# Performance work log

Measured on AMD Instinct MI355X. Metric: run time of the kernel, lower is better.

## Reference

```python
import jax, jax.numpy as jnp
import numpy as np

C = 256
CQK = C // 8  # query/key channels from Conv2d(in_dim, in_dim//8, 1)


def _cross_attn(x, y, qw, qb, kw, kb, vw, vb, gamma):
    # x, y: [B, C, H, W]; 1x1 convs are channel matmuls
    B, Cc, H, W = x.shape
    N = H * W
    xf = x.reshape(B, Cc, N)
    yf = y.reshape(B, Cc, N)
    q = jnp.einsum('oc,bcn->bno', qw, xf) + qb  # [B, N, CQK]
    k = jnp.einsum('oc,bcn->bon', kw, yf) + kb[:, None]  # [B, CQK, N]
    energy = jnp.einsum('bnc,bcm->bnm', q, k)  # [B, N, N]
    attn = jax.nn.softmax(energy, axis=2)
    v = jnp.einsum('oc,bcn->bon', vw, yf) + vb[:, None]  # [B, C, N]
    out = jnp.einsum('bcm,bnm->bcn', v, attn)  # value @ attention^T
    out = out.reshape(B, Cc, H, W)
    return gamma * out + x


def setup_inputs() -> dict:
    key = jax.random.key(0)
    ks = jax.random.split(key, 16)
    B, H, W = 4, 64, 64
    s = 1.0 / np.sqrt(C)
    d = {
        'x': jax.random.normal(ks[0], (B, C, H, W), jnp.float32),
        'y': jax.random.normal(ks[1], (B, C, H, W), jnp.float32),
        'z': jax.random.normal(ks[2], (B, C, H, W), jnp.float32),
        'q1_w': jax.random.normal(ks[3], (CQK, C), jnp.float32) * s,
        'q1_b': jax.random.normal(ks[4], (CQK,), jnp.float32) * s,
        'k1_w': jax.random.normal(ks[5], (CQK, C), jnp.float32) * s,
        'k1_b': jax.random.normal(ks[6], (CQK,), jnp.float32) * s,
        'v1_w': jax.random.normal(ks[7], (C, C), jnp.float32) * s,
        'v1_b': jax.random.normal(ks[8], (C,), jnp.float32) * s,
        'gamma1': jax.random.normal(ks[9], (1,), jnp.float32) * 0.1,
        'q2_w': jax.random.normal(ks[10], (CQK, C), jnp.float32) * s,
        'q2_b': jax.random.normal(ks[11], (CQK,), jnp.float32) * s,
        'k2_w': jax.random.normal(ks[12], (CQK, C), jnp.float32) * s,
        'k2_b': jax.random.normal(ks[13], (CQK,), jnp.float32) * s,
        'v2_w': jax.random.normal(ks[14], (C, C), jnp.float32) * s,
        'v2_b': jax.random.normal(ks[15], (C,), jnp.float32) * s,
        'gamma2': jax.random.normal(jax.random.fold_in(key, 99), (1,), jnp.float32) * 0.1,
    }
    return d


def reference(x, y, z, q1_w, q1_b, k1_w, k1_b, v1_w, v1_b, gamma1,
              q2_w, q2_b, k2_w, k2_b, v2_w, v2_b, gamma2):
    out1 = _cross_attn(x, y, q1_w, q1_b, k1_w, k1_b, v1_w, v1_b, gamma1)
    out2 = _cross_attn(out1, z, q2_w, q2_b, k2_w, k2_b, v2_w, v2_b, gamma2)
    return out2
```

## Files before the change

### kernel.cpp

```cpp
#include <hip/hip_runtime.h>
#include <hip/hip_bf16.h>

#define NSEQ 4096
#define CDIM 256
#define CQKD 32
#define LOG2E 1.4426950408889634f

typedef float v4f __attribute__((ext_vector_type(4)));
typedef float v16f __attribute__((ext_vector_type(16)));
typedef short v8s __attribute__((ext_vector_type(8)));

__device__ __forceinline__ float exp2_(float x) { return exp2f(x); }

__device__ __forceinline__ unsigned short f2bf(float x) {
  unsigned u = __builtin_bit_cast(unsigned, x);
  unsigned r = (u + 0x7FFFu + ((u >> 16) & 1u)) >> 16;
  return (unsigned short)r;
}
__device__ __forceinline__ float bf2f(unsigned short s) {
  unsigned u = ((unsigned)s) << 16;
  return __builtin_bit_cast(float, u);
}
__device__ __forceinline__ unsigned int pack_bf16(float a, float b) {
#if __has_builtin(__builtin_amdgcn_cvt_pk_bf16_f32)
  typedef __bf16 v2bf __attribute__((ext_vector_type(2)));
  v2bf r = __builtin_amdgcn_cvt_pk_bf16_f32(a, b);
  return __builtin_bit_cast(unsigned int, r);
#else
  return ((unsigned)f2bf(b) << 16) | (unsigned)f2bf(a);
#endif
}

__device__ __forceinline__ void barrier_lds() {
  __asm__ __volatile__("s_waitcnt lgkmcnt(0)\n\ts_barrier" ::: "memory");
}

__global__ __launch_bounds__(256) void convw_kernel(
    const float* __restrict__ q1w, const float* __restrict__ k1w,
    const float* __restrict__ k2w, const float* __restrict__ q2w,
    const float* __restrict__ v1w, const float* __restrict__ v2w,
    unsigned short* __restrict__ W) {
  const int s = blockIdx.x * 256 + threadIdx.x;
  const float* src;
  int o, ch0;
  size_t obase;
  float scale = 1.0f;
  if (s < 3072) {
    const int wsel = s >> 10, r = s & 1023;
    src = wsel == 0 ? q1w : (wsel == 1 ? k1w : k2w);
    const int ot = r >> 9, cb = (r >> 6) & 7, lane = r & 63;
    o = ot * 16 + (lane & 15);
    ch0 = cb * 32 + ((lane >> 4) & 3) * 8;
    obase = (size_t)wsel * 8192 + (size_t)r * 8;
  } else if (s < 19456) {
    const int s2 = s - 3072, which = s2 >> 13, r = s2 & 8191;
    src = which == 0 ? v1w : v2w;
    const int ot = r >> 9, cb = (r >> 6) & 7, lane = r & 63;
    o = ot * 16 + (lane & 15);
    ch0 = cb * 32 + ((lane >> 4) & 3) * 8;
    obase = 32768 + (size_t)which * 65536 + (size_t)r * 8;
  } else {
    const int r = s - 19456;
    src = q2w;
    const int lane = r & 63;
    o = lane & 31;
    ch0 = (r >> 6) * 16 + (lane >> 5) * 8;
    obase = 24576 + (size_t)r * 8;
    scale = LOG2E;
  }
#pragma unroll
  for (int j = 0; j < 8; ++j)
    W[obase + j] = f2bf(src[o * CDIM + ch0 + j] * scale);
}

__global__ __launch_bounds__(256) void prep_kernel(
    const float* __restrict__ x, const float* __restrict__ y,
    const float* __restrict__ z, const unsigned short* __restrict__ Wbf,
    const float* __restrict__ q1b, const float* __restrict__ k1b,
    const float* __restrict__ k2b, const float* __restrict__ v1b,
    const float* __restrict__ v2b, unsigned short* __restrict__ Q1,
    unsigned short* __restrict__ K1, unsigned short* __restrict__ K2,
    unsigned short* __restrict__ V1, unsigned short* __restrict__ V2) {
  __shared__ unsigned short t[256][72];
  __shared__ unsigned short Kt[64][40];
  const int src = blockIdx.z;
  const float* in = src == 0 ? x : (src == 1 ? y : z);
  const int b = blockIdx.y;
  const int n0 = blockIdx.x * 64;
  const int tid = threadIdx.x, lane = tid & 63, w = tid >> 6;
  const int quad = lane >> 4, r15 = lane & 15, l31 = lane & 31, lh = lane >> 5;
  const float* ip = in + (size_t)(b * CDIM) * NSEQ + n0;
  {
    const int chb = tid >> 4, c4 = (tid & 15) * 4;
#pragma unroll
    for (int p = 0; p < 16; ++p) {
      const int ch = p * 16 + chb;
      float4 v = *(const float4*)(ip + (size_t)ch * NSEQ + c4);
      uint2 pk;
      pk.x = pack_bf16(v.x, v.y);
      pk.y = pack_bf16(v.z, v.w);
      *(uint2*)&t[ch][c4] = pk;
    }
  }
  __syncthreads();
  v8s af[8];
#pragma unroll
  for (int cb = 0; cb < 8; ++cb) {
    union { unsigned short e[8]; v8s v; } u;
#pragma unroll
    for (int j = 0; j < 8; ++j) u.e[j] = t[cb * 32 + quad * 8 + j][w * 16 + r15];
    af[cb] = u.v;
  }
  const int nt = blockIdx.x * 4 + w;
  const unsigned short* Wqk = Wbf + src * 8192;
  v4f a0 = {0.f, 0.f, 0.f, 0.f}, a1 = a0;
#pragma unroll
  for (int cb = 0; cb < 8; ++cb) {
    v8s b0 = *(const v8s*)(Wqk + (size_t)cb * 512 + lane * 8);
    v8s b1 = *(const v8s*)(Wqk + (size_t)(8 + cb) * 512 + lane * 8);
    a0 = __builtin_amdgcn_mfma_f32_16x16x32_bf16(af[cb], b0, a0, 0, 0, 0);
    a1 = __builtin_amdgcn_mfma_f32_16x16x32_bf16(af[cb], b1, a1, 0, 0, 0);
  }
  if (src == 0) {
#pragma unroll
    for (int r = 0; r < 4; ++r) {
      Q1[((size_t)b * NSEQ + nt * 16 + quad * 4 + r) * CQKD + r15] =
          f2bf((a0[r] + q1b[r15]) * LOG2E);
      Q1[((size_t)b * NSEQ + nt * 16 + quad * 4 + r) * CQKD + 16 + r15] =
          f2bf((a1[r] + q1b[16 + r15]) * LOG2E);
    }
    return;
  }
  const float* kbias = src == 1 ? k1b : k2b;
#pragma unroll
  for (int r = 0; r < 4; ++r) {
    Kt[w * 16 + quad * 4 + r][r15] = f2bf(a0[r] + kbias[r15]);
    Kt[w * 16 + quad * 4 + r][16 + r15] = f2bf(a1[r] + kbias[16 + r15]);
  }
  const unsigned short* Wv = Wbf + 32768 + (src - 1) * 65536;
  const float* vbias = src == 1 ? v1b : v2b;
  v4f vacc[16];
#pragma unroll
  for (int ot = 0; ot < 16; ++ot) vacc[ot] = (v4f){0.f, 0.f, 0.f, 0.f};
#pragma unroll
  for (int cb = 0; cb < 8; ++cb) {
    const v8s afc = af[cb];
#pragma unroll
    for (int ot = 0; ot < 16; ++ot) {
      v8s bf = *(const v8s*)(Wv + (size_t)(ot * 8 + cb) * 512 + lane * 8);
      vacc[ot] = __builtin_amdgcn_mfma_f32_16x16x32_bf16(afc, bf, vacc[ot], 0, 0, 0);
    }
  }
  __syncthreads();
#pragma unroll
  for (int ot = 0; ot < 16; ++ot) {
    const int ch = ot * 16 + r15;
    const float bv = vbias[ch];
    uint2 pk;
    pk.x = pack_bf16(vacc[ot][0] + bv, vacc[ot][1] + bv);
    pk.y = pack_bf16(vacc[ot][2] + bv, vacc[ot][3] + bv);
    *(uint2*)&t[ch][w * 16 + quad * 4] = pk;
  }
  {
    unsigned short* Kout = (src == 1 ? K1 : K2) + (size_t)b * (NSEQ / 16) * 512;
    *(v8s*)(Kout + ((size_t)nt * 64 + lane) * 8) = *(const v8s*)&Kt[w * 16 + r15][quad * 8];
  }
  __syncthreads();
  unsigned short* Vout = (src == 1 ? V1 : V2) + (size_t)b * (NSEQ / 16) * 8 * 512;
#pragma unroll
  for (int chb = 0; chb < 8; ++chb)
    *(v8s*)(Vout + (((size_t)nt * 8 + chb) * 64 + lane) * 8) =
        *(const v8s*)&t[chb * 32 + l31][w * 16 + lh * 8];
}

#define PSTR 136

__device__ __forceinline__ void attn_tile(
    const unsigned short* __restrict__ Kl, const unsigned short* __restrict__ Vl,
    unsigned short* __restrict__ P, const v8s qf[4], int w, int lane,
    int pbuf, int tn, const v8s kfu, const v8s* vfu, v8s& kfn, v8s* vfn,
    v16f acc[2], float lsum[4]) {
  const v4f vzero4 = {0.f, 0.f, 0.f, 0.f};
  const int quad = (lane >> 4) & 3, r15 = lane & 15;
  const int l31 = lane & 31, lh = lane >> 5;
  kfn = *(const v8s*)(Kl + (size_t)tn * 4096);
#pragma unroll
  for (int s = 0; s < 8; ++s)
    vfn[s] = *(const v8s*)(Vl + ((size_t)tn * 64 + s * 8) * 512);
  unsigned short* pw = P + pbuf * (64 * PSTR) + w * 16 + quad * 4;
#pragma unroll
  for (int qt = 0; qt < 4; ++qt) {
    v4f st = __builtin_amdgcn_mfma_f32_16x16x32_bf16(kfu, qf[qt], vzero4, 0, 0, 0);
    float e0 = exp2_(st[0]), e1 = exp2_(st[1]), e2 = exp2_(st[2]), e3 = exp2_(st[3]);
    lsum[qt] += (e0 + e1) + (e2 + e3);
    uint2 pk;
    pk.x = pack_bf16(e0, e1);
    pk.y = pack_bf16(e2, e3);
    *(uint2*)(pw + (qt * 16 + r15) * PSTR) = pk;
  }
  barrier_lds();
  const unsigned short* pb = P + pbuf * (64 * PSTR);
#pragma unroll
  for (int s = 0; s < 8; ++s) {
    v8s pf0 = *(const v8s*)(pb + (size_t)l31 * PSTR + s * 16 + lh * 8);
    v8s pf1 = *(const v8s*)(pb + (size_t)(32 + l31) * PSTR + s * 16 + lh * 8);
    acc[0] = __builtin_amdgcn_mfma_f32_32x32x16_bf16(vfu[s], pf0, acc[0], 0, 0, 0);
    acc[1] = __builtin_amdgcn_mfma_f32_32x32x16_bf16(vfu[s], pf1, acc[1], 0, 0, 0);
  }
}

__device__ __forceinline__ void attn_loop(
    const unsigned short* __restrict__ Kp, const unsigned short* __restrict__ Vp,
    unsigned short* __restrict__ P, const v8s qf[4], int w, int lane,
    v16f acc[2], float lsum[4]) {
  const unsigned short* Kl = Kp + (size_t)w * 512 + lane * 8;
  const unsigned short* Vl = Vp + (size_t)w * 512 + lane * 8;
  v8s kA, kB, vA[8], vB[8];
  kA = *(const v8s*)(Kl);
#pragma unroll
  for (int s = 0; s < 8; ++s) vA[s] = *(const v8s*)(Vl + (size_t)s * 8 * 512);
  for (int kt = 0; kt < 32; kt += 2) {
    attn_tile(Kl, Vl, P, qf, w, lane, 0, (kt + 1) & 31, kA, vA, kB, vB, acc, lsum);
    attn_tile(Kl, Vl, P, qf, w, lane, 1, (kt + 2) & 31, kB, vB, kA, vA, acc, lsum);
  }
}

__global__ __launch_bounds__(512, 2) void fused_attn_kernel(
    const unsigned short* __restrict__ Q1g, const unsigned short* __restrict__ K1g,
    const unsigned short* __restrict__ V1g, const unsigned short* __restrict__ K2g,
    const unsigned short* __restrict__ V2g, const unsigned short* __restrict__ W2g,
    const float* __restrict__ x, const float* __restrict__ q2b,
    const float* __restrict__ g1p, const float* __restrict__ g2p,
    float* __restrict__ outp) {
  __shared__ __align__(16) unsigned short P[2 * 64 * PSTR];
  __shared__ __align__(16) unsigned short out1T[64 * 264];
  __shared__ __align__(16) unsigned short q2s[64 * 32];
  __shared__ float lbuf[8][64];

  const int tid = threadIdx.x;
  const int lane = tid & 63;
  const int w = tid >> 6;
  const int quad = lane >> 4;
  const int r15 = lane & 15;
  const int l31 = lane & 31, lh = lane >> 5;
  const int b = blockIdx.x & 3;
  const int n0 = (blockIdx.x >> 2) * 64;

  const float g1 = g1p[0];
  const float g2 = g2p[0];

  const unsigned short* Qp  = Q1g + (size_t)b * NSEQ * CQKD;
  const unsigned short* K1p = K1g + (size_t)b * (NSEQ / 16) * 512;
  const unsigned short* K2p = K2g + (size_t)b * (NSEQ / 16) * 512;
  const unsigned short* V1p = V1g + (size_t)b * (NSEQ / 16) * 8 * 512;
  const unsigned short* V2p = V2g + (size_t)b * (NSEQ / 16) * 8 * 512;

  v8s qf[4];
#pragma unroll
  for (int qt = 0; qt < 4; ++qt)
    qf[qt] = *(const v8s*)(Qp + (n0 + qt * 16 + r15) * CQKD + quad * 8);

  v16f acc[2];
  float lsum[4] = {0.f, 0.f, 0.f, 0.f};
  acc[0] = (v16f)(0.f); acc[1] = (v16f)(0.f);

  attn_loop(K1p, V1p, P, qf, w, lane, acc, lsum);
#pragma unroll
  for (int qt = 0; qt < 4; ++qt) {
    lsum[qt] += __shfl_xor(lsum[qt], 16);
    lsum[qt] += __shfl_xor(lsum[qt], 32);
  }
  if (lane < 16) {
#pragma unroll
    for (int qt = 0; qt < 4; ++qt) lbuf[w][qt * 16 + lane] = lsum[qt];
  }
  __syncthreads();
  float rinv[2];
#pragma unroll
  for (int qh = 0; qh < 2; ++qh) {
    const int q = qh * 32 + l31;
    float d = 0.f;
#pragma unroll
    for (int ww = 0; ww < 8; ++ww) d += lbuf[ww][q];
    rinv[qh] = 1.0f / d;
  }
#pragma unroll
  for (int qh = 0; qh < 2; ++qh) {
    const int q = qh * 32 + l31;
#pragma unroll
    for (int rg = 0; rg < 4; ++rg) {
      const int c = w * 32 + 8 * rg + 4 * lh;
      float o0 = g1 * (acc[qh][rg * 4 + 0] * rinv[qh]) + x[((size_t)b * CDIM + c + 0) * NSEQ + n0 + q];
      float o1 = g1 * (acc[qh][rg * 4 + 1] * rinv[qh]) + x[((size_t)b * CDIM + c + 1) * NSEQ + n0 + q];
      float o2 = g1 * (acc[qh][rg * 4 + 2] * rinv[qh]) + x[((size_t)b * CDIM + c + 2) * NSEQ + n0 + q];
      float o3 = g1 * (acc[qh][rg * 4 + 3] * rinv[qh]) + x[((size_t)b * CDIM + c + 3) * NSEQ + n0 + q];
      uint2 pk;
      pk.x = pack_bf16(o0, o1);
      pk.y = pack_bf16(o2, o3);
      *(uint2*)(out1T + (size_t)q * 264 + c) = pk;
    }
  }
  __syncthreads();

  if (w < 2) {
    const int qh = w;
    v16f qacc = (v16f)(0.f);
#pragma unroll
    for (int s = 0; s < 16; ++s) {
      v8s af = *(const v8s*)(W2g + (size_t)(s * 64 + lane) * 8);
      v8s bf = *(const v8s*)(out1T + (size_t)(qh * 32 + l31) * 264 + s * 16 + lh * 8);
      qacc = __builtin_amdgcn_mfma_f32_32x32x16_bf16(af, bf, qacc, 0, 0, 0);
    }
#pragma unroll
    for (int rg = 0; rg < 4; ++rg) {
      const int o = 8 * rg + 4 * lh;
      uint2 pk;
      pk.x = pack_bf16(qacc[rg * 4 + 0] + q2b[o + 0] * LOG2E, qacc[rg * 4 + 1] + q2b[o + 1] * LOG2E);
      pk.y = pack_bf16(qacc[rg * 4 + 2] + q2b[o + 2] * LOG2E, qacc[rg * 4 + 3] + q2b[o + 3] * LOG2E);
      *(uint2*)(q2s + (size_t)(qh * 32 + l31) * 32 + o) = pk;
    }
  }
  __syncthreads();

#pragma unroll
  for (int qt = 0; qt < 4; ++qt)
    qf[qt] = *(const v8s*)(q2s + (qt * 16 + r15) * 32 + quad * 8);
  acc[0] = (v16f)(0.f); acc[1] = (v16f)(0.f);
#pragma unroll
  for (int qt = 0; qt < 4; ++qt) lsum[qt] = 0.f;
  attn_loop(K2p, V2p, P, qf, w, lane, acc, lsum);
#pragma unroll
  for (int qt = 0; qt < 4; ++qt) {
    lsum[qt] += __shfl_xor(lsum[qt], 16);
    lsum[qt] += __shfl_xor(lsum[qt], 32);
  }
  __syncthreads();
  if (lane < 16) {
#pragma unroll
    for (int qt = 0; qt < 4; ++qt) lbuf[w][qt * 16 + lane] = lsum[qt];
  }
  __syncthreads();
#pragma unroll
  for (int qh = 0; qh < 2; ++qh) {
    const int q = qh * 32 + l31;
    float d = 0.f;
#pragma unroll
    for (int ww = 0; ww < 8; ++ww) d += lbuf[ww][q];
    rinv[qh] = 1.0f / d;
  }
#pragma unroll
  for (int qh = 0; qh < 2; ++qh) {
    const int q = qh * 32 + l31;
#pragma unroll
    for (int rg = 0; rg < 4; ++rg) {
      const int c = w * 32 + 8 * rg + 4 * lh;
#pragma unroll
      for (int i = 0; i < 4; ++i) {
        float res = bf2f(out1T[(size_t)q * 264 + c + i]);
        outp[((size_t)b * CDIM + c + i) * NSEQ + n0 + q] =
            g2 * (acc[qh][rg * 4 + i] * rinv[qh]) + res;
      }
    }
  }
}

extern "C" void kernel_launch(void* const* d_in, const int* in_sizes, int n_in,
                              void* d_out, int out_size, void* d_ws, size_t ws_size,
                              hipStream_t stream) {
  const float* x   = (const float*)d_in[0];
  const float* y   = (const float*)d_in[1];
  const float* z   = (const float*)d_in[2];
  const float* q1w = (const float*)d_in[3];
  const float* q1b = (const float*)d_in[4];
  const float* k1w = (const float*)d_in[5];
  const float* k1b = (const float*)d_in[6];
  const float* v1w = (const float*)d_in[7];
  const float* v1b = (const float*)d_in[8];
  const float* g1  = (const float*)d_in[9];
  const float* q2w = (const float*)d_in[10];
  const float* q2b = (const float*)d_in[11];
  const float* k2w = (const float*)d_in[12];
  const float* k2b = (const float*)d_in[13];
  const float* v2w = (const float*)d_in[14];
  const float* v2b = (const float*)d_in[15];
  const float* g2  = (const float*)d_in[16];
  char* ws = (char*)d_ws;
  unsigned short* Wbf = (unsigned short*)(ws);
  unsigned short* Q1  = (unsigned short*)(ws + 327680);
  unsigned short* K1  = (unsigned short*)(ws + 1376256);
  unsigned short* K2  = (unsigned short*)(ws + 2424832);
  unsigned short* V1  = (unsigned short*)(ws + 3473408);
  unsigned short* V2  = (unsigned short*)(ws + 11862016);
  float* outp = (float*)d_out;

  convw_kernel<<<dim3(80), 256, 0, stream>>>(q1w, k1w, k2w, q2w, v1w, v2w, Wbf);
  prep_kernel<<<dim3(64, 4, 3), 256, 0, stream>>>(x, y, z, Wbf, q1b, k1b, k2b, v1b,
                                                  v2b, Q1, K1, K2, V1, V2);
  fused_attn_kernel<<<dim3(256), 512, 0, stream>>>(Q1, K1, V1, K2, V2, Wbf + 24576, x,
                                                   q2b, g1, g2, outp);
}
```

Measured before the change: 237.2 us.

## Switch P·V matmul to FP8 with a max-subtraction pre-pass

Stores V and the softmax probabilities P as FP8 e4m3 and runs the P·V product with FP8 MFMA instructions instead of BF16, halving V global traffic and P LDS traffic. FP8 range is narrow, so a separate pass over the keys first computes the per-query row max, which is subtracted before exp2. exp2 now uses the hardware intrinsic. This adds a full extra QK pass per attention stage and lowers the precision of the probabilities and values, which risks accuracy tolerance.

```diff
diff --git a/kernel.cpp b/kernel.cpp
--- a/kernel.cpp
+++ b/kernel.cpp
@@ -9,8 +9,17 @@
 typedef float v4f __attribute__((ext_vector_type(4)));
 typedef float v16f __attribute__((ext_vector_type(16)));
 typedef short v8s __attribute__((ext_vector_type(8)));
-
-__device__ __forceinline__ float exp2_(float x) { return exp2f(x); }
+typedef unsigned long long u64;
+
+__device__ __forceinline__ float exp2_(float x) {
+#if __has_builtin(__builtin_amdgcn_exp2f)
+  return __builtin_amdgcn_exp2f(x);
+#else
+  float r;
+  __asm__("v_exp_f32 %0, %1" : "=v"(r) : "v"(x));
+  return r;
+#endif
+}
 
 __device__ __forceinline__ unsigned short f2bf(float x) {
   unsigned u = __builtin_bit_cast(unsigned, x);
@@ -28,6 +37,35 @@
   return __builtin_bit_cast(unsigned int, r);
 #else
   return ((unsigned)f2bf(b) << 16) | (unsigned)f2bf(a);
+#endif
+}
+
+__device__ __forceinline__ unsigned char f2e4m3(float x) {
+  unsigned u = __builtin_bit_cast(unsigned, x);
+  unsigned s = (u >> 24) & 0x80u;
+  unsigned au = u & 0x7fffffffu;
+  if (au > 0x43e00000u) return (unsigned char)(s | 0x7eu);
+  if (au < 0x3c800000u) {
+    float ax = __builtin_bit_cast(float, au);
+    int q = (int)(ax * 512.0f + 0.5f);
+    if (q > 7) q = 7;
+    return (unsigned char)(s | (unsigned)q);
+  }
+  int e = (int)((au >> 23) & 0xffu) - 127 + 7;
+  unsigned m = au & 0x7fffffu;
+  unsigned mr = m + 0x7ffffu + ((m >> 20) & 1u);
+  if (mr >= 0x800000u) { mr -= 0x800000u; e += 1; if (e >= 16) return (unsigned char)(s | 0x7e); }
+  return (unsigned char)(s | ((unsigned)e << 3) | (mr >> 20));
+}
+__device__ __forceinline__ unsigned int pack4_fp8(float a, float b, float c, float d) {
+#if __has_builtin(__builtin_amdgcn_cvt_pk_fp8_f32)
+  int v = 0;
+  v = __builtin_amdgcn_cvt_pk_fp8_f32(a, b, v, false);
+  v = __builtin_amdgcn_cvt_pk_fp8_f32(c, d, v, true);
+  return (unsigned int)v;
+#else
+  return (unsigned)f2e4m3(a) | ((unsigned)f2e4m3(b) << 8) |
+         ((unsigned)f2e4m3(c) << 16) | ((unsigned)f2e4m3(d) << 24);
 #endif
 }
 
@@ -80,7 +118,7 @@
     const float* __restrict__ k2b, const float* __restrict__ v1b,
     const float* __restrict__ v2b, unsigned short* __restrict__ Q1,
     unsigned short* __restrict__ K1, unsigned short* __restrict__ K2,
-    unsigned short* __restrict__ V1, unsigned short* __restrict__ V2) {
+    unsigned char* __restrict__ V1, unsigned char* __restrict__ V2) {
   __shared__ unsigned short t[256][72];
   __shared__ unsigned short Kt[64][40];
   const int src = blockIdx.z;
@@ -152,33 +190,69 @@
     }
   }
   __syncthreads();
+  unsigned char* Vt8 = (unsigned char*)t;
 #pragma unroll
   for (int ot = 0; ot < 16; ++ot) {
     const int ch = ot * 16 + r15;
     const float bv = vbias[ch];
-    uint2 pk;
-    pk.x = pack_bf16(vacc[ot][0] + bv, vacc[ot][1] + bv);
-    pk.y = pack_bf16(vacc[ot][2] + bv, vacc[ot][3] + bv);
-    *(uint2*)&t[ch][w * 16 + quad * 4] = pk;
+    *(unsigned int*)&Vt8[(size_t)ch * 72 + w * 16 + quad * 4] =
+        pack4_fp8(vacc[ot][0] + bv, vacc[ot][1] + bv, vacc[ot][2] + bv, vacc[ot][3] + bv);
   }
   {
     unsigned short* Kout = (src == 1 ? K1 : K2) + (size_t)b * (NSEQ / 16) * 512;
     *(v8s*)(Kout + ((size_t)nt * 64 + lane) * 8) = *(const v8s*)&Kt[w * 16 + r15][quad * 8];
   }
   __syncthreads();
-  unsigned short* Vout = (src == 1 ? V1 : V2) + (size_t)b * (NSEQ / 16) * 8 * 512;
+  unsigned char* Vout = (src == 1 ? V1 : V2) + (size_t)b * (NSEQ / 16) * 8 * 512;
 #pragma unroll
   for (int chb = 0; chb < 8; ++chb)
-    *(v8s*)(Vout + (((size_t)nt * 8 + chb) * 64 + lane) * 8) =
-        *(const v8s*)&t[chb * 32 + l31][w * 16 + lh * 8];
-}
-
-#define PSTR 136
+    *(u64*)(Vout + (((size_t)nt * 8 + chb) * 64 + lane) * 8) =
+        *(const u64*)&Vt8[(size_t)(chb * 32 + l31) * 72 + w * 16 + lh * 8];
+}
+
+
+__device__ __forceinline__ void max_pass(
+    const unsigned short* __restrict__ Kp, const v8s qf[4], int w, int lane,
+    float (*lbuf)[64], float m[4]) {
+  const v4f vzero4 = {0.f, 0.f, 0.f, 0.f};
+  const int r15 = lane & 15;
+  const unsigned short* Kl = Kp + (size_t)w * 512 + lane * 8;
+  v8s kA = *(const v8s*)(Kl);
+#pragma unroll
+  for (int qt = 0; qt < 4; ++qt) m[qt] = -3.0e38f;
+  for (int kt = 0; kt < 32; ++kt) {
+    v8s kB = *(const v8s*)(Kl + (size_t)((kt + 1) & 31) * 4096);
+#pragma unroll
+    for (int qt = 0; qt < 4; ++qt) {
+      v4f st = __builtin_amdgcn_mfma_f32_16x16x32_bf16(kA, qf[qt], vzero4, 0, 0, 0);
+      m[qt] = fmaxf(m[qt], fmaxf(fmaxf(st[0], st[1]), fmaxf(st[2], st[3])));
+    }
+    kA = kB;
+  }
+#pragma unroll
+  for (int qt = 0; qt < 4; ++qt) {
+    m[qt] = fmaxf(m[qt], __shfl_xor(m[qt], 16));
+    m[qt] = fmaxf(m[qt], __shfl_xor(m[qt], 32));
+  }
+  if (lane < 16) {
+#pragma unroll
+    for (int qt = 0; qt < 4; ++qt) lbuf[w][qt * 16 + lane] = m[qt];
+  }
+  __syncthreads();
+#pragma unroll
+  for (int qt = 0; qt < 4; ++qt) {
+    float mm = lbuf[0][qt * 16 + r15];
+#pragma unroll
+    for (int ww = 1; ww < 8; ++ww) mm = fmaxf(mm, lbuf[ww][qt * 16 + r15]);
+    m[qt] = mm;
+  }
+  __syncthreads();
+}
 
 __device__ __forceinline__ void attn_tile(
-    const unsigned short* __restrict__ Kl, const unsigned short* __restrict__ Vl,
-    unsigned short* __restrict__ P, const v8s qf[4], int w, int lane,
-    int pbuf, int tn, const v8s kfu, const v8s* vfu, v8s& kfn, v8s* vfn,
+    const unsigned short* __restrict__ Kl, const unsigned char* __restrict__ Vl,
+    unsigned char* __restrict__ P, const v8s qf[4], const float m[4], int w, int lane,
+    int pbuf, int tn, const v8s kfu, const u64* vfu, v8s& kfn, u64* vfn,
     v16f acc[2], float lsum[4]) {
   const v4f vzero4 = {0.f, 0.f, 0.f, 0.f};
   const int quad = (lane >> 4) & 3, r15 = lane & 15;
@@ -186,53 +260,52 @@
   kfn = *(const v8s*)(Kl + (size_t)tn * 4096);
 #pragma unroll
   for (int s = 0; s < 8; ++s)
-    vfn[s] = *(const v8s*)(Vl + ((size_t)tn * 64 + s * 8) * 512);
-  unsigned short* pw = P + pbuf * (64 * PSTR) + w * 16 + quad * 4;
+    vfn[s] = *(const u64*)(Vl + (size_t)tn * 32768 + s * 4096);
+  unsigned char* pw = P + pbuf * 8704 + w * 16 + quad * 4;
 #pragma unroll
   for (int qt = 0; qt < 4; ++qt) {
     v4f st = __builtin_amdgcn_mfma_f32_16x16x32_bf16(kfu, qf[qt], vzero4, 0, 0, 0);
-    float e0 = exp2_(st[0]), e1 = exp2_(st[1]), e2 = exp2_(st[2]), e3 = exp2_(st[3]);
+    float e0 = exp2_(st[0] - m[qt]), e1 = exp2_(st[1] - m[qt]);
+    float e2 = exp2_(st[2] - m[qt]), e3 = exp2_(st[3] - m[qt]);
     lsum[qt] += (e0 + e1) + (e2 + e3);
-    uint2 pk;
-    pk.x = pack_bf16(e0, e1);
-    pk.y = pack_bf16(e2, e3);
-    *(uint2*)(pw + (qt * 16 + r15) * PSTR) = pk;
+    *(unsigned int*)(pw + (size_t)(qt * 16 + r15) * 136) = pack4_fp8(e0, e1, e2, e3);
   }
   barrier_lds();
-  const unsigned short* pb = P + pbuf * (64 * PSTR);
+  const unsigned char* pb = P + pbuf * 8704;
 #pragma unroll
   for (int s = 0; s < 8; ++s) {
-    v8s pf0 = *(const v8s*)(pb + (size_t)l31 * PSTR + s * 16 + lh * 8);
-    v8s pf1 = *(const v8s*)(pb + (size_t)(32 + l31) * PSTR + s * 16 + lh * 8);
-    acc[0] = __builtin_amdgcn_mfma_f32_32x32x16_bf16(vfu[s], pf0, acc[0], 0, 0, 0);
-    acc[1] = __builtin_amdgcn_mfma_f32_32x32x16_bf16(vfu[s], pf1, acc[1], 0, 0, 0);
+    long pf0 = (long)*(const u64*)(pb + (size_t)l31 * 136 + s * 16 + lh * 8);
+    long pf1 = (long)*(const u64*)(pb + (size_t)(32 + l31) * 136 + s * 16 + lh * 8);
+    acc[0] = __builtin_amdgcn_mfma_f32_32x32x16_fp8_fp8((long)vfu[s], pf0, acc[0], 0, 0, 0);
+    acc[1] = __builtin_amdgcn_mfma_f32_32x32x16_fp8_fp8((long)vfu[s], pf1, acc[1], 0, 0, 0);
   }
 }
 
 __device__ __forceinline__ void attn_loop(
-    const unsigned short* __restrict__ Kp, const unsigned short* __restrict__ Vp,
-    unsigned short* __restrict__ P, const v8s qf[4], int w, int lane,
+    const unsigned short* __restrict__ Kp, const unsigned char* __restrict__ Vp,
+    unsigned char* __restrict__ P, const v8s qf[4], const float m[4], int w, int lane,
     v16f acc[2], float lsum[4]) {
   const unsigned short* Kl = Kp + (size_t)w * 512 + lane * 8;
-  const unsigned short* Vl = Vp + (size_t)w * 512 + lane * 8;
-  v8s kA, kB, vA[8], vB[8];
+  const unsigned char* Vl = Vp + (size_t)w * 512 + lane * 8;
+  v8s kA, kB;
+  u64 vA[8], vB[8];
   kA = *(const v8s*)(Kl);
 #pragma unroll
-  for (int s = 0; s < 8; ++s) vA[s] = *(const v8s*)(Vl + (size_t)s * 8 * 512);
+  for (int s = 0; s < 8; ++s) vA[s] = *(const u64*)(Vl + (size_t)s * 4096);
   for (int kt = 0; kt < 32; kt += 2) {
-    attn_tile(Kl, Vl, P, qf, w, lane, 0, (kt + 1) & 31, kA, vA, kB, vB, acc, lsum);
-    attn_tile(Kl, Vl, P, qf, w, lane, 1, (kt + 2) & 31, kB, vB, kA, vA, acc, lsum);
+    attn_tile(Kl, Vl, P, qf, m, w, lane, 0, (kt + 1) & 31, kA, vA, kB, vB, acc, lsum);
+    attn_tile(Kl, Vl, P, qf, m, w, lane, 1, (kt + 2) & 31, kB, vB, kA, vA, acc, lsum);
   }
 }
 
 __global__ __launch_bounds__(512, 2) void fused_attn_kernel(
     const unsigned short* __restrict__ Q1g, const unsigned short* __restrict__ K1g,
-    const unsigned short* __restrict__ V1g, const unsigned short* __restrict__ K2g,
-    const unsigned short* __restrict__ V2g, const unsigned short* __restrict__ W2g,
+    const unsigned char* __restrict__ V1g, const unsigned short* __restrict__ K2g,
+    const unsigned char* __restrict__ V2g, const unsigned short* __restrict__ W2g,
     const float* __restrict__ x, const float* __restrict__ q2b,
     const float* __restrict__ g1p, const float* __restrict__ g2p,
     float* __restrict__ outp) {
-  __shared__ __align__(16) unsigned short P[2 * 64 * PSTR];
+  __shared__ __align__(16) unsigned char P[2 * 8704];
   __shared__ __align__(16) unsigned short out1T[64 * 264];
   __shared__ __align__(16) unsigned short q2s[64 * 32];
   __shared__ float lbuf[8][64];
@@ -252,8 +325,8 @@
   const unsigned short* Qp  = Q1g + (size_t)b * NSEQ * CQKD;
   const unsigned short* K1p = K1g + (size_t)b * (NSEQ / 16) * 512;
   const unsigned short* K2p = K2g + (size_t)b * (NSEQ / 16) * 512;
-  const unsigned short* V1p = V1g + (size_t)b * (NSEQ / 16) * 8 * 512;
-  const unsigned short* V2p = V2g + (size_t)b * (NSEQ / 16) * 8 * 512;
+  const unsigned char* V1p  = V1g + (size_t)b * (NSEQ / 16) * 8 * 512;
+  const unsigned char* V2p  = V2g + (size_t)b * (NSEQ / 16) * 8 * 512;
 
   v8s qf[4];
 #pragma unroll
@@ -262,14 +335,17 @@
 
   v16f acc[2];
   float lsum[4] = {0.f, 0.f, 0.f, 0.f};
+  float m[4];
   acc[0] = (v16f)(0.f); acc[1] = (v16f)(0.f);
 
-  attn_loop(K1p, V1p, P, qf, w, lane, acc, lsum);
+  max_pass(K1p, qf, w, lane, lbuf, m);
+  attn_loop(K1p, V1p, P, qf, m, w, lane, acc, lsum);
 #pragma unroll
   for (int qt = 0; qt < 4; ++qt) {
     lsum[qt] += __shfl_xor(lsum[qt], 16);
     lsum[qt] += __shfl_xor(lsum[qt], 32);
   }
+  __syncthreads();
   if (lane < 16) {
 #pragma unroll
     for (int qt = 0; qt < 4; ++qt) lbuf[w][qt * 16 + lane] = lsum[qt];
@@ -328,7 +404,8 @@
   acc[0] = (v16f)(0.f); acc[1] = (v16f)(0.f);
 #pragma unroll
   for (int qt = 0; qt < 4; ++qt) lsum[qt] = 0.f;
-  attn_loop(K2p, V2p, P, qf, w, lane, acc, lsum);
+  max_pass(K2p, qf, w, lane, lbuf, m);
+  attn_loop(K2p, V2p, P, qf, m, w, lane, acc, lsum);
 #pragma unroll
   for (int qt = 0; qt < 4; ++qt) {
     lsum[qt] += __shfl_xor(lsum[qt], 16);
@@ -389,8 +466,8 @@
   unsigned short* Q1  = (unsigned short*)(ws + 327680);
   unsigned short* K1  = (unsigned short*)(ws + 1376256);
   unsigned short* K2  = (unsigned short*)(ws + 2424832);
-  unsigned short* V1  = (unsigned short*)(ws + 3473408);
-  unsigned short* V2  = (unsigned short*)(ws + 11862016);
+  unsigned char*  V1  = (unsigned char*)(ws + 3473408);
+  unsigned char*  V2  = (unsigned char*)(ws + 7667712);
   float* outp = (float*)d_out;
 
   convw_kernel<<<dim3(80), 256, 0, stream>>>(q1w, k1w, k2w, q2w, v1w, v2w, Wbf);
```

After: 222.1 us. -6.4%, faster.
